# Optimization experiments

Measured on AMD Instinct MI355X. Metric: run time of the kernel, lower is better.

The kernel has to match this reference:

```python
import jax, jax.numpy as jnp
import numpy as np

E, M, K, INTER = 8, 4096, 2048, 5632
N = 2 * INTER  # gate + up projections fused in w1
TOPK = 2


def setup_inputs() -> dict:
    key = jax.random.key(0)
    k1, k2, k3, k4, k5 = jax.random.split(key, 5)
    a1 = jax.random.normal(k1, (M, K), dtype=jnp.float32)
    w1 = jax.random.normal(k2, (E, N, K), dtype=jnp.float32) * (K ** -0.5)
    w2 = jax.random.normal(k3, (E, K, INTER), dtype=jnp.float32) * (INTER ** -0.5)
    topk_weights = jax.random.uniform(k4, (M, TOPK), dtype=jnp.float32)
    topk_ids = jax.random.randint(k5, (M, TOPK), 0, E, dtype=jnp.int64)
    return {"a1": a1, "w1": w1, "w2": w2,
            "topk_weights": topk_weights, "topk_ids": topk_ids}


def reference(a1, w1, w2, topk_weights, topk_ids):
    # Fused MoE: dispatch (identity/unquantized path) -> per-expert
    # SwiGLU expert GEMMs -> weighted combine over top-k routing.
    n_half = w1.shape[1] // 2
    fused = jnp.zeros((a1.shape[0], topk_ids.shape[1], w2.shape[1]), a1.dtype)  # [M, topk, K]
    for e in range(w1.shape[0]):  # small fixed expert count
        h = jnp.einsum('mk,nk->mn', a1, w1[e])          # [M, N]
        act = jax.nn.silu(h[:, :n_half]) * h[:, n_half:]  # [M, N/2]
        o = jnp.einsum('mn,kn->mk', act, w2[e])          # [M, K]
        mask = (topk_ids == e).astype(a1.dtype)          # [M, topk]
        fused = fused + mask[..., None] * o[:, None, :]
    # combine: weighted reduction over topk -> output [M, K]
    return jnp.einsum('mt,mtk->mk', topk_weights, fused)
```

## Files before the change

### kernel.cpp

```cpp
#include <hip/hip_runtime.h>
#include <hip/hip_bf16.h>

#define NEXP   8
#define MTOK   4096
#define KDIM   2048
#define NINTER 5632
#define NPAIR  8192

#define AS3 __attribute__((address_space(3)))
#define AS1 __attribute__((address_space(1)))

typedef __attribute__((ext_vector_type(4))) float f32x4;
typedef __attribute__((ext_vector_type(8))) short s16x8;

#define MEMFENCE asm volatile("" ::: "memory")
#define SB       __builtin_amdgcn_s_barrier()
#define SCHEDB   __builtin_amdgcn_sched_barrier(0)
#define WAITV8   asm volatile("s_waitcnt vmcnt(8)" ::: "memory")
#define WAITV0   asm volatile("s_waitcnt vmcnt(0)" ::: "memory")
#define WAITLG   asm volatile("s_waitcnt lgkmcnt(0)" ::: "memory")

__device__ __forceinline__ short f2bf(float f) {
  union { float f; unsigned u; } v; v.f = f;
  unsigned r = v.u + 0x7FFFu + ((v.u >> 16) & 1u);
  return (short)(r >> 16);
}

__device__ __forceinline__ s16x8 pack8(float4 a, float4 b) {
  s16x8 v;
  v[0] = f2bf(a.x); v[1] = f2bf(a.y); v[2] = f2bf(a.z); v[3] = f2bf(a.w);
  v[4] = f2bf(b.x); v[5] = f2bf(b.y); v[6] = f2bf(b.z); v[7] = f2bf(b.w);
  return v;
}

__global__ __launch_bounds__(256) void cvt_k(const float* __restrict__ src,
                                             unsigned short* __restrict__ dst, size_t n8) {
  size_t i = (size_t)blockIdx.x * blockDim.x + threadIdx.x;
  size_t stride = (size_t)gridDim.x * blockDim.x;
  for (; i < n8; i += stride) {
    const float4* p = (const float4*)(src + i * 8);
    float4 f0 = p[0], f1 = p[1];
    *(s16x8*)(dst + i * 8) = pack8(f0, f1);
  }
}

__global__ __launch_bounds__(512) void route_k(const int* __restrict__ ids,
                                               int* __restrict__ off,
                                               int* __restrict__ list) {
  __shared__ int sids[NPAIR];
  __shared__ int scnt[64][8];
  __shared__ int sstart[64][8];
  __shared__ int s_is64;
  int tid = threadIdx.x;
  if (tid == 0) s_is64 = 1;
  __syncthreads();
  for (int i = tid; i < NPAIR / 2; i += 512)
    if (ids[2 * i + 1] != 0) s_is64 = 0;
  __syncthreads();
  int is64 = s_is64;
  for (int i = tid; i < NPAIR; i += 512) {
    int e = is64 ? ids[2 * i] : ids[i];
    if (e < 0) e = 0; if (e > 7) e = 7;
    sids[i] = e;
  }
  if (tid < 64)
    for (int e = 0; e < 8; ++e) scnt[tid][e] = 0;
  __syncthreads();
  if (tid < 64) {
    int b0 = tid * 128;
    for (int i = 0; i < 128; ++i) ++scnt[tid][sids[b0 + i]];
  }
  __syncthreads();
  if (tid == 0) {
    int tot = 0;
    for (int e = 0; e < 8; ++e) {
      off[e] = tot;
      for (int c = 0; c < 64; ++c) { sstart[c][e] = tot; tot += scnt[c][e]; }
    }
    off[8] = tot;
  }
  __syncthreads();
  if (tid < 64) {
    int b0 = tid * 128;
    for (int i = 0; i < 128; ++i) {
      int p = b0 + i;
      int e = sids[p];
      list[sstart[tid][e]++] = p;
    }
  }
}

__global__ __launch_bounds__(512, 2) void gemm1_k8(const float* __restrict__ w2f,
                                                   unsigned short* __restrict__ w2b,
                                                   const unsigned short* __restrict__ a1b,
                                                   const unsigned short* __restrict__ w1b,
                                                   const int* __restrict__ off,
                                                   const int* __restrict__ list,
                                                   unsigned short* __restrict__ act) {
  extern __shared__ __align__(16) char smem[];
  short* sm = (short*)smem;
  int* srow = (int*)(sm + 65536);

  int tid = threadIdx.x;
  {
    size_t bid = blockIdx.x + (size_t)gridDim.x * (blockIdx.y + (size_t)gridDim.y * blockIdx.z);
    size_t g = bid * 1024 + tid;
    if (g < 11534336u) {
      const float4* s = (const float4*)(w2f + g * 8);
      float4 f0 = s[0], f1 = s[1];
      *(s16x8*)(w2b + g * 8) = pack8(f0, f1);
    }
    g += 512;
    if (g < 11534336u) {
      const float4* s = (const float4*)(w2f + g * 8);
      float4 f0 = s[0], f1 = s[1];
      *(s16x8*)(w2b + g * 8) = pack8(f0, f1);
    }
  }

  int e = blockIdx.z, mt = blockIdx.y, nt = blockIdx.x;
  int base = off[e];
  int cnt  = off[e + 1] - base;
  if (mt * 256 >= cnt) return;

  for (int i = tid; i < 256; i += 512) {
    int r = mt * 256 + i;
    srow[i] = (r < cnt) ? (list[base + r] >> 1) : (list[base + cnt - 1] >> 1);
  }
  __syncthreads();

  int lane = tid & 63, w = tid >> 6;
  int wm = w >> 2, wn = w & 3;
  int lrow = lane & 15, lhi = lane >> 4;
  int l8 = lane >> 3, c8 = lane & 7;

  f32x4 accg[8][2], accu[8][2];
#pragma unroll
  for (int i = 0; i < 8; ++i)
#pragma unroll
    for (int j = 0; j < 2; ++j) { accg[i][j] = (f32x4)(0.f); accu[i][j] = (f32x4)(0.f); }

  const unsigned short* w1be = w1b + (size_t)e * (2 * NINTER) * KDIM;
  const unsigned short* sA[4];
  const unsigned short* sG[2];
  int aD[4], bD[2];
#pragma unroll
  for (int q = 0; q < 4; ++q) {
    int r = q * 64 + w * 8 + l8;
    sA[q] = a1b + (size_t)srow[r] * KDIM + ((c8 ^ (r & 7)) * 8);
    aD[q] = (q * 64 + w * 8) * 64;
  }
#pragma unroll
  for (int q = 0; q < 2; ++q) {
    int r = q * 64 + w * 8 + l8;
    sG[q] = w1be + (size_t)(nt * 128 + r) * KDIM + ((c8 ^ (r & 7)) * 8);
    bD[q] = (q * 64 + w * 8) * 64;
  }
  const size_t UPOFF = (size_t)NINTER * KDIM;

  auto STAGE = [&](int t, int b) {
    int ko = t * 64;
#pragma unroll
    for (int q = 0; q < 4; ++q)
      __builtin_amdgcn_global_load_lds((const AS1 void*)(sA[q] + ko), (AS3 void*)(sm + b * 16384 + aD[q]), 16, 0, 0);
#pragma unroll
    for (int q = 0; q < 2; ++q) {
      __builtin_amdgcn_global_load_lds((const AS1 void*)(sG[q] + ko), (AS3 void*)(sm + 32768 + b * 8192 + bD[q]), 16, 0, 0);
      __builtin_amdgcn_global_load_lds((const AS1 void*)(sG[q] + UPOFF + ko), (AS3 void*)(sm + 49152 + b * 8192 + bD[q]), 16, 0, 0);
    }
  };

  STAGE(0, 0);
  STAGE(1, 1);
  WAITV8; SCHEDB; MEMFENCE; SB; MEMFENCE; SCHEDB;

  int b = 0;
  for (int t = 0; t < KDIM / 64; ++t) {
    s16x8 aL[4][2], bg[2][2], bu[2][2];
#pragma unroll
    for (int i = 0; i < 4; ++i)
#pragma unroll
      for (int kk = 0; kk < 2; ++kk) {
        int r = wm * 128 + i * 16 + lrow, ch = kk * 4 + lhi;
        aL[i][kk] = *(const s16x8*)&sm[b * 16384 + r * 64 + ((ch ^ (r & 7)) * 8)];
      }
#pragma unroll
    for (int j = 0; j < 2; ++j)
#pragma unroll
      for (int kk = 0; kk < 2; ++kk) {
        int r = wn * 32 + j * 16 + lrow, ch = kk * 4 + lhi;
        bg[j][kk] = *(const s16x8*)&sm[32768 + b * 8192 + r * 64 + ((ch ^ (r & 7)) * 8)];
        bu[j][kk] = *(const s16x8*)&sm[49152 + b * 8192 + r * 64 + ((ch ^ (r & 7)) * 8)];
      }
    __builtin_amdgcn_s_setprio(1);
#pragma unroll
    for (int i = 0; i < 4; ++i)
#pragma unroll
      for (int j = 0; j < 2; ++j)
#pragma unroll
        for (int kk = 0; kk < 2; ++kk) {
          accg[i][j] = __builtin_amdgcn_mfma_f32_16x16x32_bf16(aL[i][kk], bg[j][kk], accg[i][j], 0, 0, 0);
          accu[i][j] = __builtin_amdgcn_mfma_f32_16x16x32_bf16(aL[i][kk], bu[j][kk], accu[i][j], 0, 0, 0);
        }
    __builtin_amdgcn_s_setprio(0);
#pragma unroll
    for (int i = 0; i < 4; ++i)
#pragma unroll
      for (int kk = 0; kk < 2; ++kk) {
        int r = wm * 128 + (i + 4) * 16 + lrow, ch = kk * 4 + lhi;
        aL[i][kk] = *(const s16x8*)&sm[b * 16384 + r * 64 + ((ch ^ (r & 7)) * 8)];
      }
    __builtin_amdgcn_s_setprio(1);
#pragma unroll
    for (int i = 0; i < 4; ++i)
#pragma unroll
      for (int j = 0; j < 2; ++j)
#pragma unroll
        for (int kk = 0; kk < 2; ++kk) {
          accg[i + 4][j] = __builtin_amdgcn_mfma_f32_16x16x32_bf16(aL[i][kk], bg[j][kk], accg[i + 4][j], 0, 0, 0);
          accu[i + 4][j] = __builtin_amdgcn_mfma_f32_16x16x32_bf16(aL[i][kk], bu[j][kk], accu[i + 4][j], 0, 0, 0);
        }
    __builtin_amdgcn_s_setprio(0);

    WAITLG; SCHEDB; MEMFENCE; SB; MEMFENCE; SCHEDB;
    if (t + 2 < KDIM / 64) {
      STAGE(t + 2, b);
      WAITV8;
    } else {
      WAITV0;
    }
    SCHEDB; MEMFENCE; SB; MEMFENCE; SCHEDB;
    b ^= 1;
  }

#pragma unroll
  for (int i = 0; i < 8; ++i) {
#pragma unroll
    for (int q = 0; q < 4; ++q) {
      int grow = mt * 256 + wm * 128 + i * 16 + lhi * 4 + q;
      if (grow < cnt) {
        size_t rowoff = (size_t)(base + grow) * NINTER;
#pragma unroll
        for (int j = 0; j < 2; ++j) {
          float g = accg[i][j][q], u = accu[i][j][q];
          float a = (g / (1.f + __expf(-g))) * u;
          int col = nt * 128 + wn * 32 + j * 16 + lrow;
          act[rowoff + col] = (unsigned short)f2bf(a);
        }
      }
    }
  }
}

__global__ __launch_bounds__(512, 2) void gemm2_k8(const unsigned short* __restrict__ act,
                                                   const unsigned short* __restrict__ w2b,
                                                   const int* __restrict__ off,
                                                   const int* __restrict__ list,
                                                   const float* __restrict__ tw,
                                                   float* __restrict__ out) {
  extern __shared__ __align__(16) char smem[];
  short* sm = (short*)smem;

  int e = blockIdx.z, mt = blockIdx.y, nt = blockIdx.x;
  int base = off[e];
  int cnt  = off[e + 1] - base;
  if (mt * 256 >= cnt) return;

  int tid = threadIdx.x;
  int lane = tid & 63, w = tid >> 6;
  int wm = w >> 2, wn = w & 3;
  int lrow = lane & 15, lhi = lane >> 4;
  int l8 = lane >> 3, c8 = lane & 7;

  f32x4 acc[8][4];
#pragma unroll
  for (int i = 0; i < 8; ++i)
#pragma unroll
    for (int j = 0; j < 4; ++j) acc[i][j] = (f32x4)(0.f);

  const unsigned short* w2be = w2b + (size_t)e * KDIM * NINTER;
  const unsigned short* sA[4];
  const unsigned short* sB[4];
  int dOf[4];
#pragma unroll
  for (int q = 0; q < 4; ++q) {
    int r = q * 64 + w * 8 + l8;
    int g = mt * 256 + r; if (g >= cnt) g = cnt - 1;
    int swz = (c8 ^ (r & 7)) * 8;
    sA[q] = act + (size_t)(base + g) * NINTER + swz;
    sB[q] = w2be + (size_t)(nt * 256 + r) * NINTER + swz;
    dOf[q] = (q * 64 + w * 8) * 64;
  }

  auto STAGE = [&](int t, int b) {
    int ko = t * 64;
#pragma unroll
    for (int q = 0; q < 4; ++q)
      __builtin_amdgcn_global_load_lds((const AS1 void*)(sA[q] + ko), (AS3 void*)(sm + b * 16384 + dOf[q]), 16, 0, 0);
#pragma unroll
    for (int q = 0; q < 4; ++q)
      __builtin_amdgcn_global_load_lds((const AS1 void*)(sB[q] + ko), (AS3 void*)(sm + 32768 + b * 16384 + dOf[q]), 16, 0, 0);
  };

  STAGE(0, 0);
  STAGE(1, 1);
  WAITV8; SCHEDB; MEMFENCE; SB; MEMFENCE; SCHEDB;

  int b = 0;
  for (int t = 0; t < NINTER / 64; ++t) {
    s16x8 aL[4][2], bb[4][2];
#pragma unroll
    for (int i = 0; i < 4; ++i)
#pragma unroll
      for (int kk = 0; kk < 2; ++kk) {
        int r = wm * 128 + i * 16 + lrow, ch = kk * 4 + lhi;
        aL[i][kk] = *(const s16x8*)&sm[b * 16384 + r * 64 + ((ch ^ (r & 7)) * 8)];
      }
#pragma unroll
    for (int j = 0; j < 4; ++j)
#pragma unroll
      for (int kk = 0; kk < 2; ++kk) {
        int r = wn * 64 + j * 16 + lrow, ch = kk * 4 + lhi;
        bb[j][kk] = *(const s16x8*)&sm[32768 + b * 16384 + r * 64 + ((ch ^ (r & 7)) * 8)];
      }
    __builtin_amdgcn_s_setprio(1);
#pragma unroll
    for (int i = 0; i < 4; ++i)
#pragma unroll
      for (int j = 0; j < 4; ++j)
#pragma unroll
        for (int kk = 0; kk < 2; ++kk)
          acc[i][j] = __builtin_amdgcn_mfma_f32_16x16x32_bf16(aL[i][kk], bb[j][kk], acc[i][j], 0, 0, 0);
    __builtin_amdgcn_s_setprio(0);
#pragma unroll
    for (int i = 0; i < 4; ++i)
#pragma unroll
      for (int kk = 0; kk < 2; ++kk) {
        int r = wm * 128 + (i + 4) * 16 + lrow, ch = kk * 4 + lhi;
        aL[i][kk] = *(const s16x8*)&sm[b * 16384 + r * 64 + ((ch ^ (r & 7)) * 8)];
      }
    __builtin_amdgcn_s_setprio(1);
#pragma unroll
    for (int i = 0; i < 4; ++i)
#pragma unroll
      for (int j = 0; j < 4; ++j)
#pragma unroll
        for (int kk = 0; kk < 2; ++kk)
          acc[i + 4][j] = __builtin_amdgcn_mfma_f32_16x16x32_bf16(aL[i][kk], bb[j][kk], acc[i + 4][j], 0, 0, 0);
    __builtin_amdgcn_s_setprio(0);

    WAITLG; SCHEDB; MEMFENCE; SB; MEMFENCE; SCHEDB;
    if (t + 2 < NINTER / 64) {
      STAGE(t + 2, b);
      WAITV8;
    } else {
      WAITV0;
    }
    SCHEDB; MEMFENCE; SB; MEMFENCE; SCHEDB;
    b ^= 1;
  }

#pragma unroll
  for (int i = 0; i < 8; ++i) {
#pragma unroll
    for (int q = 0; q < 4; ++q) {
      int grow = mt * 256 + wm * 128 + i * 16 + lhi * 4 + q;
      if (grow < cnt) {
        int p = list[base + grow];
        int m = p >> 1;
        float wgt = tw[p];
#pragma unroll
        for (int j = 0; j < 4; ++j) {
          int col = nt * 256 + wn * 64 + j * 16 + lrow;
          atomicAdd(&out[(size_t)m * KDIM + col], wgt * acc[i][j][q]);
        }
      }
    }
  }
}

__global__ __launch_bounds__(256, 2) void gemm1_fb(const float* __restrict__ a1,
                                                   const float* __restrict__ w1,
                                                   const int* __restrict__ off,
                                                   const int* __restrict__ list,
                                                   unsigned short* __restrict__ act) {
  int e = blockIdx.z, mt = blockIdx.y, nt = blockIdx.x;
  int base = off[e];
  int cnt  = off[e + 1] - base;
  if (mt * 128 >= cnt) return;
  __shared__ __align__(16) short lA[128 * 64];
  __shared__ __align__(16) short lBg[128 * 64];
  __shared__ __align__(16) short lBu[128 * 64];
  __shared__ int srow[128];
  int tid = threadIdx.x;
  if (tid < 128) {
    int r = mt * 128 + tid;
    srow[tid] = (r < cnt) ? (list[base + r] >> 1) : 0;
  }
  __syncthreads();
  int lane = tid & 63, wave = tid >> 6;
  int wm = wave >> 1, wn = wave & 1;
  int lrow = lane & 15, lhi = lane >> 4;
  f32x4 accg[4][4], accu[4][4];
#pragma unroll
  for (int i = 0; i < 4; ++i)
#pragma unroll
    for (int j = 0; j < 4; ++j) { accg[i][j] = (f32x4)(0.f); accu[i][j] = (f32x4)(0.f); }
  const float* w1e = w1 + (size_t)e * (2 * NINTER) * KDIM;
  int n0 = nt * 128;
  for (int k0 = 0; k0 < KDIM; k0 += 64) {
#pragma unroll
    for (int c4 = 0; c4 < 4; ++c4) {
      int cid = c4 * 256 + tid;
      int row = cid >> 3, k8 = cid & 7;
      const float* s = a1 + (size_t)srow[row] * KDIM + k0 + k8 * 8;
      float4 f0 = *(const float4*)s;
      float4 f1 = *(const float4*)(s + 4);
      *(s16x8*)&lA[row * 64 + ((k8 ^ (row & 7)) * 8)] = pack8(f0, f1);
    }
#pragma unroll
    for (int c4 = 0; c4 < 4; ++c4) {
      int cid = c4 * 256 + tid;
      int row = cid >> 3, k8 = cid & 7;
      const float* sg = w1e + (size_t)(n0 + row) * KDIM + k0 + k8 * 8;
      const float* su = w1e + (size_t)(NINTER + n0 + row) * KDIM + k0 + k8 * 8;
      float4 g0 = *(const float4*)sg;
      float4 g1 = *(const float4*)(sg + 4);
      float4 u0 = *(const float4*)su;
      float4 u1 = *(const float4*)(su + 4);
      int o = row * 64 + ((k8 ^ (row & 7)) * 8);
      *(s16x8*)&lBg[o] = pack8(g0, g1);
      *(s16x8*)&lBu[o] = pack8(u0, u1);
    }
    __syncthreads();
#pragma unroll
    for (int kk = 0; kk < 2; ++kk) {
      s16x8 af[4], bg[4], bu[4];
      int chunk = kk * 4 + lhi;
#pragma unroll
      for (int i = 0; i < 4; ++i) {
        int r = wm * 64 + i * 16 + lrow;
        af[i] = *(const s16x8*)&lA[r * 64 + ((chunk ^ (r & 7)) * 8)];
      }
#pragma unroll
      for (int j = 0; j < 4; ++j) {
        int r = wn * 64 + j * 16 + lrow;
        int o = r * 64 + ((chunk ^ (r & 7)) * 8);
        bg[j] = *(const s16x8*)&lBg[o];
        bu[j] = *(const s16x8*)&lBu[o];
      }
#pragma unroll
      for (int i = 0; i < 4; ++i)
#pragma unroll
        for (int j = 0; j < 4; ++j) {
          accg[i][j] = __builtin_amdgcn_mfma_f32_16x16x32_bf16(af[i], bg[j], accg[i][j], 0, 0, 0);
          accu[i][j] = __builtin_amdgcn_mfma_f32_16x16x32_bf16(af[i], bu[j], accu[i][j], 0, 0, 0);
        }
    }
    __syncthreads();
  }
#pragma unroll
  for (int i = 0; i < 4; ++i) {
#pragma unroll
    for (int q = 0; q < 4; ++q) {
      int r = wm * 64 + i * 16 + lhi * 4 + q;
      int grow = mt * 128 + r;
      if (grow < cnt) {
        size_t rowoff = (size_t)(base + grow) * NINTER;
#pragma unroll
        for (int j = 0; j < 4; ++j) {
          float g = accg[i][j][q], u = accu[i][j][q];
          float a = (g / (1.f + __expf(-g))) * u;
          int col = n0 + wn * 64 + j * 16 + lrow;
          act[rowoff + col] = (unsigned short)f2bf(a);
        }
      }
    }
  }
}

__global__ __launch_bounds__(256, 2) void gemm2_fb(const unsigned short* __restrict__ act,
                                                   const float* __restrict__ w2,
                                                   const int* __restrict__ off,
                                                   const int* __restrict__ list,
                                                   const float* __restrict__ tw,
                                                   float* __restrict__ out) {
  int e = blockIdx.z, mt = blockIdx.y, nt = blockIdx.x;
  int base = off[e];
  int cnt  = off[e + 1] - base;
  if (mt * 128 >= cnt) return;
  __shared__ __align__(16) short lA[128 * 64];
  __shared__ __align__(16) short lB[128 * 64];
  int tid = threadIdx.x;
  int lane = tid & 63, wave = tid >> 6;
  int wm = wave >> 1, wn = wave & 1;
  int lrow = lane & 15, lhi = lane >> 4;
  f32x4 acc[4][4];
#pragma unroll
  for (int i = 0; i < 4; ++i)
#pragma unroll
    for (int j = 0; j < 4; ++j) acc[i][j] = (f32x4)(0.f);
  const float* w2e = w2 + (size_t)e * KDIM * NINTER;
  for (int k0 = 0; k0 < NINTER; k0 += 64) {
#pragma unroll
    for (int c4 = 0; c4 < 4; ++c4) {
      int cid = c4 * 256 + tid;
      int row = cid >> 3, k8 = cid & 7;
      int grow = mt * 128 + row;
      if (grow >= cnt) grow = cnt - 1;
      s16x8 v = *(const s16x8*)(act + (size_t)(base + grow) * NINTER + k0 + k8 * 8);
      *(s16x8*)&lA[row * 64 + ((k8 ^ (row & 7)) * 8)] = v;
    }
#pragma unroll
    for (int c4 = 0; c4 < 4; ++c4) {
      int cid = c4 * 256 + tid;
      int row = cid >> 3, k8 = cid & 7;
      const float* s = w2e + (size_t)(nt * 128 + row) * NINTER + k0 + k8 * 8;
      float4 f0 = *(const float4*)s;
      float4 f1 = *(const float4*)(s + 4);
      *(s16x8*)&lB[row * 64 + ((k8 ^ (row & 7)) * 8)] = pack8(f0, f1);
    }
    __syncthreads();
#pragma unroll
    for (int kk = 0; kk < 2; ++kk) {
      s16x8 af[4], bf[4];
      int chunk = kk * 4 + lhi;
#pragma unroll
      for (int i = 0; i < 4; ++i) {
        int r = wm * 64 + i * 16 + lrow;
        af[i] = *(const s16x8*)&lA[r * 64 + ((chunk ^ (r & 7)) * 8)];
      }
#pragma unroll
      for (int j = 0; j < 4; ++j) {
        int r = wn * 64 + j * 16 + lrow;
        bf[j] = *(const s16x8*)&lB[r * 64 + ((chunk ^ (r & 7)) * 8)];
      }
#pragma unroll
      for (int i = 0; i < 4; ++i)
#pragma unroll
        for (int j = 0; j < 4; ++j)
          acc[i][j] = __builtin_amdgcn_mfma_f32_16x16x32_bf16(af[i], bf[j], acc[i][j], 0, 0, 0);
    }
    __syncthreads();
  }
#pragma unroll
  for (int i = 0; i < 4; ++i) {
#pragma unroll
    for (int q = 0; q < 4; ++q) {
      int r = wm * 64 + i * 16 + lhi * 4 + q;
      int grow = mt * 128 + r;
      if (grow < cnt) {
        int p = list[base + grow];
        int m = p >> 1;
        float wgt = tw[p];
#pragma unroll
        for (int j = 0; j < 4; ++j) {
          int col = nt * 128 + wn * 64 + j * 16 + lrow;
          atomicAdd(&out[(size_t)m * KDIM + col], wgt * acc[i][j][q]);
        }
      }
    }
  }
}

extern "C" void kernel_launch(void* const* d_in, const int* in_sizes, int n_in,
                              void* d_out, int out_size, void* d_ws, size_t ws_size,
                              hipStream_t stream) {
  const float* a1 = (const float*)d_in[0];
  const float* w1 = (const float*)d_in[1];
  const float* w2 = (const float*)d_in[2];
  const float* tw = (const float*)d_in[3];
  const int*   ids = (const int*)d_in[4];
  float* out = (float*)d_out;

  int* off  = (int*)d_ws;
  int* list = off + 16;
  unsigned short* act = (unsigned short*)((char*)d_ws + 65536);
  size_t actB = (size_t)NPAIR * NINTER * 2;
  unsigned short* a1b = (unsigned short*)((char*)act + actB);
  size_t a1B = (size_t)MTOK * KDIM * 2;
  unsigned short* w1b = (unsigned short*)((char*)a1b + a1B);
  size_t w1B = (size_t)NEXP * 2 * NINTER * KDIM * 2;
  unsigned short* w2b = (unsigned short*)((char*)w1b + w1B);
  size_t w2B = (size_t)NEXP * KDIM * NINTER * 2;
  size_t need = 65536 + actB + a1B + w1B + w2B;

  hipMemsetAsync(d_out, 0, (size_t)MTOK * KDIM * sizeof(float), stream);
  route_k<<<1, 512, 0, stream>>>(ids, off, list);

  if (ws_size >= need) {
    hipFuncSetAttribute((const void*)gemm1_k8, hipFuncAttributeMaxDynamicSharedMemorySize, 132096);
    hipFuncSetAttribute((const void*)gemm2_k8, hipFuncAttributeMaxDynamicSharedMemorySize, 131072);
    cvt_k<<<2048, 256, 0, stream>>>(a1, a1b, (size_t)MTOK * KDIM / 8);
    cvt_k<<<2048, 256, 0, stream>>>(w1, w1b, (size_t)NEXP * 2 * NINTER * KDIM / 8);
    gemm1_k8<<<dim3(NINTER / 128, 32, NEXP), 512, 132096, stream>>>(w2, w2b, a1b, w1b, off, list, act);
    gemm2_k8<<<dim3(KDIM / 256, 32, NEXP), 512, 131072, stream>>>(act, w2b, off, list, tw, out);
  } else {
    gemm1_fb<<<dim3(NINTER / 128, 64, NEXP), 256, 0, stream>>>(a1, w1, off, list, act);
    gemm2_fb<<<dim3(KDIM / 128, 64, NEXP), 256, 0, stream>>>(act, w2, off, list, tw, out);
  }
}
```

Baseline: 1.187 ms.

## Interleave LDS prefetch with MFMA quadrants in both expert GEMM main loops

Both grouped GEMM kernels are restructured into a ping-pong schedule. Each K-step is split into four MFMA quadrants, and global-to-LDS loads for the next tiles are issued between quadrants with finer barriers and lgkmcnt/vmcnt waits, replacing the old load-everything-then-compute loop. gemm1 also changes its warp layout from 2x4 to 4x2 with 64x64 warp tiles, moves srow into static shared memory, and runs the fused w2 fp32-to-bf16 conversion after the GEMM, unguarded. The aim is better overlap of memory traffic with matrix-core work, at the cost of many more barriers per iteration.

```diff
diff --git a/kernel.cpp b/kernel.cpp
--- a/kernel.cpp
+++ b/kernel.cpp
@@ -13,12 +13,15 @@
 typedef __attribute__((ext_vector_type(4))) float f32x4;
 typedef __attribute__((ext_vector_type(8))) short s16x8;
 
-#define MEMFENCE asm volatile("" ::: "memory")
-#define SB       __builtin_amdgcn_s_barrier()
-#define SCHEDB   __builtin_amdgcn_sched_barrier(0)
-#define WAITV8   asm volatile("s_waitcnt vmcnt(8)" ::: "memory")
-#define WAITV0   asm volatile("s_waitcnt vmcnt(0)" ::: "memory")
-#define WAITLG   asm volatile("s_waitcnt lgkmcnt(0)" ::: "memory")
+#define MEMF   asm volatile("" ::: "memory")
+#define BARX   do { MEMF; __builtin_amdgcn_s_barrier(); MEMF; } while (0)
+#define SCHEDB __builtin_amdgcn_sched_barrier(0)
+#define WAITV6 asm volatile("s_waitcnt vmcnt(6)" ::: "memory")
+#define WAITV0 asm volatile("s_waitcnt vmcnt(0)" ::: "memory")
+#define LG8    asm volatile("s_waitcnt lgkmcnt(8)" ::: "memory")
+#define LG0    asm volatile("s_waitcnt lgkmcnt(0)" ::: "memory")
+#define PRIO1  __builtin_amdgcn_s_setprio(1)
+#define PRIO0  __builtin_amdgcn_s_setprio(0)
 
 __device__ __forceinline__ short f2bf(float f) {
   union { float f; unsigned u; } v; v.f = f;
@@ -99,156 +102,192 @@
                                                    unsigned short* __restrict__ act) {
   extern __shared__ __align__(16) char smem[];
   short* sm = (short*)smem;
-  int* srow = (int*)(sm + 65536);
-
-  int tid = threadIdx.x;
-  {
-    size_t bid = blockIdx.x + (size_t)gridDim.x * (blockIdx.y + (size_t)gridDim.y * blockIdx.z);
-    size_t g = bid * 1024 + tid;
-    if (g < 11534336u) {
-      const float4* s = (const float4*)(w2f + g * 8);
-      float4 f0 = s[0], f1 = s[1];
-      *(s16x8*)(w2b + g * 8) = pack8(f0, f1);
-    }
-    g += 512;
-    if (g < 11534336u) {
-      const float4* s = (const float4*)(w2f + g * 8);
-      float4 f0 = s[0], f1 = s[1];
-      *(s16x8*)(w2b + g * 8) = pack8(f0, f1);
-    }
-  }
+  __shared__ int srow[256];
 
   int e = blockIdx.z, mt = blockIdx.y, nt = blockIdx.x;
   int base = off[e];
   int cnt  = off[e + 1] - base;
-  if (mt * 256 >= cnt) return;
-
-  for (int i = tid; i < 256; i += 512) {
-    int r = mt * 256 + i;
-    srow[i] = (r < cnt) ? (list[base + r] >> 1) : (list[base + cnt - 1] >> 1);
-  }
-  __syncthreads();
-
-  int lane = tid & 63, w = tid >> 6;
-  int wm = w >> 2, wn = w & 3;
-  int lrow = lane & 15, lhi = lane >> 4;
-  int l8 = lane >> 3, c8 = lane & 7;
-
-  f32x4 accg[8][2], accu[8][2];
-#pragma unroll
-  for (int i = 0; i < 8; ++i)
-#pragma unroll
-    for (int j = 0; j < 2; ++j) { accg[i][j] = (f32x4)(0.f); accu[i][j] = (f32x4)(0.f); }
-
-  const unsigned short* w1be = w1b + (size_t)e * (2 * NINTER) * KDIM;
-  const unsigned short* sA[4];
-  const unsigned short* sG[2];
-  int aD[4], bD[2];
-#pragma unroll
-  for (int q = 0; q < 4; ++q) {
-    int r = q * 64 + w * 8 + l8;
-    sA[q] = a1b + (size_t)srow[r] * KDIM + ((c8 ^ (r & 7)) * 8);
-    aD[q] = (q * 64 + w * 8) * 64;
-  }
-#pragma unroll
-  for (int q = 0; q < 2; ++q) {
-    int r = q * 64 + w * 8 + l8;
-    sG[q] = w1be + (size_t)(nt * 128 + r) * KDIM + ((c8 ^ (r & 7)) * 8);
-    bD[q] = (q * 64 + w * 8) * 64;
-  }
-  const size_t UPOFF = (size_t)NINTER * KDIM;
-
-  auto STAGE = [&](int t, int b) {
-    int ko = t * 64;
-#pragma unroll
-    for (int q = 0; q < 4; ++q)
-      __builtin_amdgcn_global_load_lds((const AS1 void*)(sA[q] + ko), (AS3 void*)(sm + b * 16384 + aD[q]), 16, 0, 0);
-#pragma unroll
-    for (int q = 0; q < 2; ++q) {
-      __builtin_amdgcn_global_load_lds((const AS1 void*)(sG[q] + ko), (AS3 void*)(sm + 32768 + b * 8192 + bD[q]), 16, 0, 0);
-      __builtin_amdgcn_global_load_lds((const AS1 void*)(sG[q] + UPOFF + ko), (AS3 void*)(sm + 49152 + b * 8192 + bD[q]), 16, 0, 0);
-    }
-  };
-
-  STAGE(0, 0);
-  STAGE(1, 1);
-  WAITV8; SCHEDB; MEMFENCE; SB; MEMFENCE; SCHEDB;
-
-  int b = 0;
-  for (int t = 0; t < KDIM / 64; ++t) {
-    s16x8 aL[4][2], bg[2][2], bu[2][2];
+  int tid = threadIdx.x;
+  bool work = (mt * 256 < cnt);
+
+  if (work) {
+    for (int i = tid; i < 256; i += 512) {
+      int r = mt * 256 + i;
+      srow[i] = (r < cnt) ? (list[base + r] >> 1) : (list[base + cnt - 1] >> 1);
+    }
+    __syncthreads();
+
+    int lane = tid & 63, w = tid >> 6;
+    int wm = w >> 1, wn = w & 1;
+    int lrow = lane & 15, lhi = lane >> 4;
+    int l8 = lane >> 3, c8 = lane & 7;
+
+    f32x4 accg[4][4], accu[4][4];
 #pragma unroll
     for (int i = 0; i < 4; ++i)
 #pragma unroll
-      for (int kk = 0; kk < 2; ++kk) {
-        int r = wm * 128 + i * 16 + lrow, ch = kk * 4 + lhi;
-        aL[i][kk] = *(const s16x8*)&sm[b * 16384 + r * 64 + ((ch ^ (r & 7)) * 8)];
-      }
-#pragma unroll
-    for (int j = 0; j < 2; ++j)
-#pragma unroll
-      for (int kk = 0; kk < 2; ++kk) {
-        int r = wn * 32 + j * 16 + lrow, ch = kk * 4 + lhi;
-        bg[j][kk] = *(const s16x8*)&sm[32768 + b * 8192 + r * 64 + ((ch ^ (r & 7)) * 8)];
-        bu[j][kk] = *(const s16x8*)&sm[49152 + b * 8192 + r * 64 + ((ch ^ (r & 7)) * 8)];
-      }
-    __builtin_amdgcn_s_setprio(1);
-#pragma unroll
-    for (int i = 0; i < 4; ++i)
-#pragma unroll
-      for (int j = 0; j < 2; ++j)
+      for (int j = 0; j < 4; ++j) { accg[i][j] = (f32x4)(0.f); accu[i][j] = (f32x4)(0.f); }
+
+    const unsigned short* w1be = w1b + (size_t)e * (2 * NINTER) * KDIM;
+    int swz = (c8 ^ l8) * 8;
+    const unsigned short* sA[4]; int aD[4];
+    const unsigned short* sG[2]; int gD[2];
+    const unsigned short* sU[2]; int uD[2];
+#pragma unroll
+    for (int u = 0; u < 4; ++u) {
+      int r = u * 64 + w * 8 + l8;
+      sA[u] = a1b + (size_t)srow[r] * KDIM + swz;
+      aD[u] = (u * 64 + w * 8) * 64;
+    }
+#pragma unroll
+    for (int u = 0; u < 2; ++u) {
+      int r = u * 64 + w * 8 + l8;
+      sG[u] = w1be + (size_t)(nt * 128 + r) * KDIM + swz;
+      sU[u] = w1be + (size_t)(NINTER + nt * 128 + r) * KDIM + swz;
+      gD[u] = 16384 + (u * 64 + w * 8) * 64;
+      uD[u] = 24576 + (u * 64 + w * 8) * 64;
+    }
+
+    auto STA = [&](int u, int d, int t) {
+      __builtin_amdgcn_global_load_lds((const AS1 void*)(sA[u] + t * 64), (AS3 void*)(sm + d * 32768 + aD[u]), 16, 0, 0);
+    };
+    auto STG = [&](int u, int d, int t) {
+      __builtin_amdgcn_global_load_lds((const AS1 void*)(sG[u] + t * 64), (AS3 void*)(sm + d * 32768 + gD[u]), 16, 0, 0);
+    };
+    auto STU = [&](int u, int d, int t) {
+      __builtin_amdgcn_global_load_lds((const AS1 void*)(sU[u] + t * 64), (AS3 void*)(sm + d * 32768 + uD[u]), 16, 0, 0);
+    };
+    auto LDA = [&](int d, int i0, s16x8 (&af)[2][2]) {
+#pragma unroll
+      for (int ii = 0; ii < 2; ++ii)
 #pragma unroll
         for (int kk = 0; kk < 2; ++kk) {
-          accg[i][j] = __builtin_amdgcn_mfma_f32_16x16x32_bf16(aL[i][kk], bg[j][kk], accg[i][j], 0, 0, 0);
-          accu[i][j] = __builtin_amdgcn_mfma_f32_16x16x32_bf16(aL[i][kk], bu[j][kk], accu[i][j], 0, 0, 0);
-        }
-    __builtin_amdgcn_s_setprio(0);
-#pragma unroll
-    for (int i = 0; i < 4; ++i)
-#pragma unroll
-      for (int kk = 0; kk < 2; ++kk) {
-        int r = wm * 128 + (i + 4) * 16 + lrow, ch = kk * 4 + lhi;
-        aL[i][kk] = *(const s16x8*)&sm[b * 16384 + r * 64 + ((ch ^ (r & 7)) * 8)];
-      }
-    __builtin_amdgcn_s_setprio(1);
-#pragma unroll
-    for (int i = 0; i < 4; ++i)
-#pragma unroll
-      for (int j = 0; j < 2; ++j)
+          int r = wm * 64 + i0 * 32 + ii * 16 + lrow, ch = kk * 4 + lhi;
+          af[ii][kk] = *(const s16x8*)&sm[d * 32768 + r * 64 + ((ch ^ (r & 7)) * 8)];
+        }
+    };
+    auto LDG = [&](int d, s16x8 (&bf)[4][2]) {
+#pragma unroll
+      for (int jj = 0; jj < 4; ++jj)
 #pragma unroll
         for (int kk = 0; kk < 2; ++kk) {
-          accg[i + 4][j] = __builtin_amdgcn_mfma_f32_16x16x32_bf16(aL[i][kk], bg[j][kk], accg[i + 4][j], 0, 0, 0);
-          accu[i + 4][j] = __builtin_amdgcn_mfma_f32_16x16x32_bf16(aL[i][kk], bu[j][kk], accu[i + 4][j], 0, 0, 0);
-        }
-    __builtin_amdgcn_s_setprio(0);
-
-    WAITLG; SCHEDB; MEMFENCE; SB; MEMFENCE; SCHEDB;
-    if (t + 2 < KDIM / 64) {
-      STAGE(t + 2, b);
-      WAITV8;
-    } else {
-      WAITV0;
-    }
-    SCHEDB; MEMFENCE; SB; MEMFENCE; SCHEDB;
-    b ^= 1;
-  }
-
-#pragma unroll
-  for (int i = 0; i < 8; ++i) {
-#pragma unroll
-    for (int q = 0; q < 4; ++q) {
-      int grow = mt * 256 + wm * 128 + i * 16 + lhi * 4 + q;
-      if (grow < cnt) {
-        size_t rowoff = (size_t)(base + grow) * NINTER;
-#pragma unroll
-        for (int j = 0; j < 2; ++j) {
-          float g = accg[i][j][q], u = accu[i][j][q];
-          float a = (g / (1.f + __expf(-g))) * u;
-          int col = nt * 128 + wn * 32 + j * 16 + lrow;
-          act[rowoff + col] = (unsigned short)f2bf(a);
-        }
-      }
-    }
+          int r = wn * 64 + jj * 16 + lrow, ch = kk * 4 + lhi;
+          bf[jj][kk] = *(const s16x8*)&sm[d * 32768 + 16384 + r * 64 + ((ch ^ (r & 7)) * 8)];
+        }
+    };
+    auto LDU = [&](int d, s16x8 (&bf)[4][2]) {
+#pragma unroll
+      for (int jj = 0; jj < 4; ++jj)
+#pragma unroll
+        for (int kk = 0; kk < 2; ++kk) {
+          int r = wn * 64 + jj * 16 + lrow, ch = kk * 4 + lhi;
+          bf[jj][kk] = *(const s16x8*)&sm[d * 32768 + 24576 + r * 64 + ((ch ^ (r & 7)) * 8)];
+        }
+    };
+    auto QG = [&](int i0, s16x8 (&af)[2][2], s16x8 (&bf)[4][2]) {
+#pragma unroll
+      for (int ii = 0; ii < 2; ++ii)
+#pragma unroll
+        for (int jj = 0; jj < 4; ++jj)
+#pragma unroll
+          for (int kk = 0; kk < 2; ++kk)
+            accg[i0 * 2 + ii][jj] = __builtin_amdgcn_mfma_f32_16x16x32_bf16(af[ii][kk], bf[jj][kk], accg[i0 * 2 + ii][jj], 0, 0, 0);
+    };
+    auto QU = [&](int i0, s16x8 (&af)[2][2], s16x8 (&bf)[4][2]) {
+#pragma unroll
+      for (int ii = 0; ii < 2; ++ii)
+#pragma unroll
+        for (int jj = 0; jj < 4; ++jj)
+#pragma unroll
+          for (int kk = 0; kk < 2; ++kk)
+            accu[i0 * 2 + ii][jj] = __builtin_amdgcn_mfma_f32_16x16x32_bf16(af[ii][kk], bf[jj][kk], accu[i0 * 2 + ii][jj], 0, 0, 0);
+    };
+
+    STA(0, 0, 0); STA(1, 0, 0); STA(2, 0, 0); STA(3, 0, 0);
+    STG(0, 0, 0); STG(1, 0, 0); STU(0, 0, 0); STU(1, 0, 0);
+    STG(0, 1, 1); STG(1, 1, 1); STU(0, 1, 1); STU(1, 1, 1);
+    STA(0, 1, 1); STA(1, 1, 1);
+    WAITV6; SCHEDB;
+    BARX;
+
+    const int NI = (KDIM / 64) / 2;
+#pragma unroll 1
+    for (int I = 0; I < NI; ++I) {
+      int t = 2 * I;
+      bool pf = (I + 1 < NI);
+      s16x8 af[2][2], bg[4][2], bu[4][2];
+      LDA(0, 0, af); LDG(0, bg);
+      STA(2, 1, t + 1); STA(3, 1, t + 1);
+      LG8; BARX; LG0; SCHEDB;
+      PRIO1; QG(0, af, bg); PRIO0;
+      BARX;
+      LDU(0, bu);
+      if (pf) { STG(0, 0, t + 2); STG(1, 0, t + 2); }
+      BARX; LG0; SCHEDB;
+      PRIO1; QU(0, af, bu); PRIO0;
+      BARX;
+      LDA(0, 1, af);
+      if (pf) { STU(0, 0, t + 2); STU(1, 0, t + 2); }
+      BARX; LG0; SCHEDB;
+      PRIO1; QG(1, af, bg); PRIO0;
+      BARX;
+      if (pf) { STA(0, 0, t + 2); STA(1, 0, t + 2); }
+      BARX;
+      PRIO1; QU(1, af, bu); PRIO0;
+      if (pf) { WAITV6; } else { WAITV0; }
+      SCHEDB;
+      BARX;
+      LDA(1, 0, af); LDG(1, bg);
+      if (pf) { STA(2, 0, t + 2); STA(3, 0, t + 2); }
+      LG8; BARX; LG0; SCHEDB;
+      PRIO1; QG(0, af, bg); PRIO0;
+      BARX;
+      LDU(1, bu);
+      if (pf) { STG(0, 1, t + 3); STG(1, 1, t + 3); }
+      BARX; LG0; SCHEDB;
+      PRIO1; QU(0, af, bu); PRIO0;
+      BARX;
+      LDA(1, 1, af);
+      if (pf) { STU(0, 1, t + 3); STU(1, 1, t + 3); }
+      BARX; LG0; SCHEDB;
+      PRIO1; QG(1, af, bg); PRIO0;
+      BARX;
+      if (pf) { STA(0, 1, t + 3); STA(1, 1, t + 3); }
+      BARX;
+      PRIO1; QU(1, af, bu); PRIO0;
+      if (pf) { WAITV6; SCHEDB; }
+      BARX;
+    }
+
+#pragma unroll
+    for (int i = 0; i < 4; ++i) {
+#pragma unroll
+      for (int q = 0; q < 4; ++q) {
+        int grow = mt * 256 + wm * 64 + i * 16 + lhi * 4 + q;
+        if (grow < cnt) {
+          size_t rowoff = (size_t)(base + grow) * NINTER;
+#pragma unroll
+          for (int j = 0; j < 4; ++j) {
+            float g = accg[i][j][q], u = accu[i][j][q];
+            float a = (g / (1.f + __expf(-g))) * u;
+            int col = nt * 128 + wn * 64 + j * 16 + lrow;
+            act[rowoff + col] = (unsigned short)f2bf(a);
+          }
+        }
+      }
+    }
+  }
+
+  {
+    size_t bid = blockIdx.x + 44u * (blockIdx.y + 32u * blockIdx.z);
+    size_t g = bid * 1024 + tid;
+    const float4* s = (const float4*)(w2f + g * 8);
+    float4 f0 = s[0], f1 = s[1];
+    *(s16x8*)(w2b + g * 8) = pack8(f0, f1);
+    g += 512;
+    s = (const float4*)(w2f + g * 8);
+    f0 = s[0]; f1 = s[1];
+    *(s16x8*)(w2b + g * 8) = pack8(f0, f1);
   }
 }
 
@@ -279,85 +318,107 @@
     for (int j = 0; j < 4; ++j) acc[i][j] = (f32x4)(0.f);
 
   const unsigned short* w2be = w2b + (size_t)e * KDIM * NINTER;
-  const unsigned short* sA[4];
-  const unsigned short* sB[4];
-  int dOf[4];
-#pragma unroll
-  for (int q = 0; q < 4; ++q) {
-    int r = q * 64 + w * 8 + l8;
+  int swz = (c8 ^ l8) * 8;
+  const unsigned short* sA[4]; const unsigned short* sB[4];
+  int aD[4], bD[4];
+#pragma unroll
+  for (int u = 0; u < 4; ++u) {
+    int r = u * 64 + w * 8 + l8;
     int g = mt * 256 + r; if (g >= cnt) g = cnt - 1;
-    int swz = (c8 ^ (r & 7)) * 8;
-    sA[q] = act + (size_t)(base + g) * NINTER + swz;
-    sB[q] = w2be + (size_t)(nt * 256 + r) * NINTER + swz;
-    dOf[q] = (q * 64 + w * 8) * 64;
-  }
-
-  auto STAGE = [&](int t, int b) {
-    int ko = t * 64;
-#pragma unroll
-    for (int q = 0; q < 4; ++q)
-      __builtin_amdgcn_global_load_lds((const AS1 void*)(sA[q] + ko), (AS3 void*)(sm + b * 16384 + dOf[q]), 16, 0, 0);
-#pragma unroll
-    for (int q = 0; q < 4; ++q)
-      __builtin_amdgcn_global_load_lds((const AS1 void*)(sB[q] + ko), (AS3 void*)(sm + 32768 + b * 16384 + dOf[q]), 16, 0, 0);
+    sA[u] = act + (size_t)(base + g) * NINTER + swz;
+    sB[u] = w2be + (size_t)(nt * 256 + r) * NINTER + swz;
+    aD[u] = (u * 64 + w * 8) * 64;
+    bD[u] = 16384 + (u * 64 + w * 8) * 64;
+  }
+
+  auto STA = [&](int u, int d, int t) {
+    __builtin_amdgcn_global_load_lds((const AS1 void*)(sA[u] + t * 64), (AS3 void*)(sm + d * 32768 + aD[u]), 16, 0, 0);
   };
-
-  STAGE(0, 0);
-  STAGE(1, 1);
-  WAITV8; SCHEDB; MEMFENCE; SB; MEMFENCE; SCHEDB;
-
-  int b = 0;
-  for (int t = 0; t < NINTER / 64; ++t) {
-    s16x8 aL[4][2], bb[4][2];
-#pragma unroll
-    for (int i = 0; i < 4; ++i)
+  auto STB = [&](int u, int d, int t) {
+    __builtin_amdgcn_global_load_lds((const AS1 void*)(sB[u] + t * 64), (AS3 void*)(sm + d * 32768 + bD[u]), 16, 0, 0);
+  };
+  auto LDA = [&](int d, int i0, s16x8 (&af)[4][2]) {
+#pragma unroll
+    for (int ii = 0; ii < 4; ++ii)
 #pragma unroll
       for (int kk = 0; kk < 2; ++kk) {
-        int r = wm * 128 + i * 16 + lrow, ch = kk * 4 + lhi;
-        aL[i][kk] = *(const s16x8*)&sm[b * 16384 + r * 64 + ((ch ^ (r & 7)) * 8)];
-      }
-#pragma unroll
-    for (int j = 0; j < 4; ++j)
+        int r = wm * 128 + i0 * 64 + ii * 16 + lrow, ch = kk * 4 + lhi;
+        af[ii][kk] = *(const s16x8*)&sm[d * 32768 + r * 64 + ((ch ^ (r & 7)) * 8)];
+      }
+  };
+  auto LDB = [&](int d, int j0, s16x8 (&bf)[2][2]) {
+#pragma unroll
+    for (int jj = 0; jj < 2; ++jj)
 #pragma unroll
       for (int kk = 0; kk < 2; ++kk) {
-        int r = wn * 64 + j * 16 + lrow, ch = kk * 4 + lhi;
-        bb[j][kk] = *(const s16x8*)&sm[32768 + b * 16384 + r * 64 + ((ch ^ (r & 7)) * 8)];
-      }
-    __builtin_amdgcn_s_setprio(1);
-#pragma unroll
-    for (int i = 0; i < 4; ++i)
-#pragma unroll
-      for (int j = 0; j < 4; ++j)
+        int r = wn * 64 + j0 * 32 + jj * 16 + lrow, ch = kk * 4 + lhi;
+        bf[jj][kk] = *(const s16x8*)&sm[d * 32768 + 16384 + r * 64 + ((ch ^ (r & 7)) * 8)];
+      }
+  };
+  auto QUAD = [&](int i0, int j0, s16x8 (&af)[4][2], s16x8 (&bf)[2][2]) {
+#pragma unroll
+    for (int ii = 0; ii < 4; ++ii)
+#pragma unroll
+      for (int jj = 0; jj < 2; ++jj)
 #pragma unroll
         for (int kk = 0; kk < 2; ++kk)
-          acc[i][j] = __builtin_amdgcn_mfma_f32_16x16x32_bf16(aL[i][kk], bb[j][kk], acc[i][j], 0, 0, 0);
-    __builtin_amdgcn_s_setprio(0);
-#pragma unroll
-    for (int i = 0; i < 4; ++i)
-#pragma unroll
-      for (int kk = 0; kk < 2; ++kk) {
-        int r = wm * 128 + (i + 4) * 16 + lrow, ch = kk * 4 + lhi;
-        aL[i][kk] = *(const s16x8*)&sm[b * 16384 + r * 64 + ((ch ^ (r & 7)) * 8)];
-      }
-    __builtin_amdgcn_s_setprio(1);
-#pragma unroll
-    for (int i = 0; i < 4; ++i)
-#pragma unroll
-      for (int j = 0; j < 4; ++j)
-#pragma unroll
-        for (int kk = 0; kk < 2; ++kk)
-          acc[i + 4][j] = __builtin_amdgcn_mfma_f32_16x16x32_bf16(aL[i][kk], bb[j][kk], acc[i + 4][j], 0, 0, 0);
-    __builtin_amdgcn_s_setprio(0);
-
-    WAITLG; SCHEDB; MEMFENCE; SB; MEMFENCE; SCHEDB;
-    if (t + 2 < NINTER / 64) {
-      STAGE(t + 2, b);
-      WAITV8;
-    } else {
-      WAITV0;
-    }
-    SCHEDB; MEMFENCE; SB; MEMFENCE; SCHEDB;
-    b ^= 1;
+          acc[i0 * 4 + ii][j0 * 2 + jj] = __builtin_amdgcn_mfma_f32_16x16x32_bf16(af[ii][kk], bf[jj][kk], acc[i0 * 4 + ii][j0 * 2 + jj], 0, 0, 0);
+  };
+
+  STA(0, 0, 0); STA(1, 0, 0); STA(2, 0, 0); STA(3, 0, 0);
+  STB(0, 0, 0); STB(1, 0, 0); STB(2, 0, 0); STB(3, 0, 0);
+  STA(0, 1, 1); STA(1, 1, 1); STA(2, 1, 1); STA(3, 1, 1);
+  STB(0, 1, 1); STB(1, 1, 1);
+  WAITV6; SCHEDB;
+  BARX;
+
+  const int NI = (NINTER / 64) / 2;
+#pragma unroll 1
+  for (int I = 0; I < NI; ++I) {
+    int t = 2 * I;
+    bool pf = (I + 1 < NI);
+    s16x8 af[4][2], b0[2][2], b1[2][2];
+    LDA(0, 0, af); LDB(0, 0, b0);
+    STB(2, 1, t + 1); STB(3, 1, t + 1);
+    LG8; BARX; LG0; SCHEDB;
+    PRIO1; QUAD(0, 0, af, b0); PRIO0;
+    BARX;
+    LDB(0, 1, b1);
+    if (pf) { STA(0, 0, t + 2); STA(2, 0, t + 2); }
+    BARX; LG0; SCHEDB;
+    PRIO1; QUAD(0, 1, af, b1); PRIO0;
+    BARX;
+    LDA(0, 1, af);
+    if (pf) { STB(0, 0, t + 2); STB(1, 0, t + 2); }
+    BARX; LG0; SCHEDB;
+    PRIO1; QUAD(1, 0, af, b0); PRIO0;
+    BARX;
+    if (pf) { STA(1, 0, t + 2); STA(3, 0, t + 2); }
+    BARX;
+    PRIO1; QUAD(1, 1, af, b1); PRIO0;
+    if (pf) { WAITV6; } else { WAITV0; }
+    SCHEDB;
+    BARX;
+    LDA(1, 0, af); LDB(1, 0, b0);
+    if (pf) { STB(2, 0, t + 2); STB(3, 0, t + 2); }
+    LG8; BARX; LG0; SCHEDB;
+    PRIO1; QUAD(0, 0, af, b0); PRIO0;
+    BARX;
+    LDB(1, 1, b1);
+    if (pf) { STA(0, 1, t + 3); STA(2, 1, t + 3); }
+    BARX; LG0; SCHEDB;
+    PRIO1; QUAD(0, 1, af, b1); PRIO0;
+    BARX;
+    LDA(1, 1, af);
+    if (pf) { STB(0, 1, t + 3); STB(1, 1, t + 3); }
+    BARX; LG0; SCHEDB;
+    PRIO1; QUAD(1, 0, af, b0); PRIO0;
+    BARX;
+    if (pf) { STA(1, 1, t + 3); STA(3, 1, t + 3); }
+    BARX;
+    PRIO1; QUAD(1, 1, af, b1); PRIO0;
+    if (pf) { WAITV6; SCHEDB; }
+    BARX;
   }
 
 #pragma unroll
@@ -589,11 +650,11 @@
   route_k<<<1, 512, 0, stream>>>(ids, off, list);
 
   if (ws_size >= need) {
-    hipFuncSetAttribute((const void*)gemm1_k8, hipFuncAttributeMaxDynamicSharedMemorySize, 132096);
+    hipFuncSetAttribute((const void*)gemm1_k8, hipFuncAttributeMaxDynamicSharedMemorySize, 131072);
     hipFuncSetAttribute((const void*)gemm2_k8, hipFuncAttributeMaxDynamicSharedMemorySize, 131072);
     cvt_k<<<2048, 256, 0, stream>>>(a1, a1b, (size_t)MTOK * KDIM / 8);
     cvt_k<<<2048, 256, 0, stream>>>(w1, w1b, (size_t)NEXP * 2 * NINTER * KDIM / 8);
-    gemm1_k8<<<dim3(NINTER / 128, 32, NEXP), 512, 132096, stream>>>(w2, w2b, a1b, w1b, off, list, act);
+    gemm1_k8<<<dim3(NINTER / 128, 32, NEXP), 512, 131072, stream>>>(w2, w2b, a1b, w1b, off, list, act);
     gemm2_k8<<<dim3(KDIM / 256, 32, NEXP), 512, 131072, stream>>>(act, w2b, off, list, tw, out);
   } else {
     gemm1_fb<<<dim3(NINTER / 128, 64, NEXP), 256, 0, stream>>>(a1, w1, off, list, act);
```

Measured after the change: 1.825 ms. 53.7% more time.
